# Optimization experiments

Hardware: AMD Instinct MI355X
Metric: run time of the kernel (lower is better)

## Reference

```python
import jax, jax.numpy as jnp
import numpy as np

TEMP = 0.7
TOPK_RATIO = 0.75
BN_EPS = 1e-5  # eval-mode BN with running_mean=0, running_var=1


def conv3x3(x, w):
    # x: [N,C,H,W], w: [O,I,3,3], stride 1, pad 1
    return jax.lax.conv_general_dilated(x, w, (1, 1), 'SAME',
                                        dimension_numbers=('NCHW', 'OIHW', 'NCHW'))


def bn(x, g, b):
    scale = g / jnp.sqrt(1.0 + BN_EPS)
    return x * scale[:, None, None] + b[:, None, None]


def glu(x):
    c = x.shape[1] // 2
    return x[:, :c] * jax.nn.sigmoid(x[:, c:])


def resblock(x, w1, g1, b1, w2, g2, b2):
    out = glu(bn(conv3x3(x, w1), g1, b1))
    out = bn(conv3x3(out, w2), g2, b2)
    return out + x


def refined_attention(h_code, word_embs, w_ctx, mask):
    B, C, H, W = h_code.shape
    Q = H * W
    S = word_embs.shape[2]
    # conv_context is a 1x1 conv (no bias): pure channel projection
    sourceT = jnp.einsum('oc,bcs->bos', w_ctx, word_embs)   # [B, idf, S]
    target = h_code.reshape(B, C, Q)                        # [B, idf, Q]
    attn = jnp.einsum('bcq,bcs->bqs', target, sourceT)      # [B, Q, S]
    attn = attn.reshape(B * Q, S) / TEMP
    # faithful to torch: mask.repeat(queryL, 1) tiles mask over rows
    mask_exp = jnp.tile(mask, (Q, 1))                       # [B*Q, S]
    attn = jnp.where(mask_exp, -jnp.inf, attn)
    if TOPK_RATIO < 1.0 and S > 1:
        k = max(1, int(S * TOPK_RATIO))
        topk_vals, _ = jax.lax.top_k(attn, k)               # sorted desc
        threshold = topk_vals[:, -1:]                       # min of top-k
        attn = jnp.where(attn < threshold, -jnp.inf, attn)
    p = jax.nn.softmax(attn, axis=1)
    nan_rows = jnp.any(jnp.isnan(p), axis=1, keepdims=True)
    p = jnp.where(nan_rows, 1.0 / S, p)                     # uniform fallback
    p = p.reshape(B, Q, S)
    attn_t = jnp.swapaxes(p, 1, 2)                          # [B, S, Q]
    wctx = jnp.einsum('bos,bsq->boq', sourceT, attn_t).reshape(B, C, H, W)
    att_map = attn_t.reshape(B, S, H, W)
    return wctx, att_map


def upsample2x(x):
    return jnp.repeat(jnp.repeat(x, 2, axis=2), 2, axis=3)


def reference(h_code, c_code, word_embs, w_ctx,
              r0_w1, r0_g1, r0_b1, r0_w2, r0_g2, r0_b2,
              r1_w1, r1_g1, r1_b1, r1_w2, r1_g2, r1_b2,
              up_w, up_g, up_b, mask):
    # c_code is in the signature of NEXT_STAGE_G.forward but unused (as in AttnGAN)
    c_code_att, att = refined_attention(h_code, word_embs, w_ctx, mask)
    h_c = jnp.concatenate([h_code, c_code_att], axis=1)     # [B, 2*ngf, H, W]
    out = resblock(h_c, r0_w1, r0_g1, r0_b1, r0_w2, r0_g2, r0_b2)
    out = resblock(out, r1_w1, r1_g1, r1_b1, r1_w2, r1_g2, r1_b2)
    # upBlock: nearest upsample x2 -> conv3x3(2ngf, 2ngf) -> BN -> GLU -> ngf
    out = glu(bn(conv3x3(upsample2x(out), up_w), up_g, up_b))
    return out, att


def setup_inputs() -> dict:
    key = jax.random.key(0)
    ks = jax.random.split(key, 24)
    B, ngf, H, W = 8, 64, 128, 128
    nef, ncf, S = 256, 100, 32
    C2 = 2 * ngf  # 128
    std = 0.02
    inp = {
        'h_code': jax.random.normal(ks[0], (B, ngf, H, W), jnp.float32),
        'c_code': jax.random.normal(ks[1], (B, ncf), jnp.float32),
        'word_embs': jax.random.normal(ks[2], (B, nef, S), jnp.float32),
        'mask': jax.random.randint(ks[3], (B, S), 0, 2).astype(bool),
        'w_ctx': jax.random.normal(ks[4], (ngf, nef), jnp.float32) * std,
    }
    for i, base in enumerate([5, 11]):
        inp[f'r{i}_w1'] = jax.random.normal(ks[base + 0], (2 * C2, C2, 3, 3), jnp.float32) * std
        inp[f'r{i}_g1'] = jnp.ones((2 * C2,), jnp.float32)
        inp[f'r{i}_b1'] = jnp.zeros((2 * C2,), jnp.float32)
        inp[f'r{i}_w2'] = jax.random.normal(ks[base + 3], (C2, C2, 3, 3), jnp.float32) * std
        inp[f'r{i}_g2'] = jnp.ones((C2,), jnp.float32)
        inp[f'r{i}_b2'] = jnp.zeros((C2,), jnp.float32)
    inp['up_w'] = jax.random.normal(ks[17], (2 * ngf, C2, 3, 3), jnp.float32) * std
    inp['up_g'] = jnp.ones((2 * ngf,), jnp.float32)
    inp['up_b'] = jnp.zeros((2 * ngf,), jnp.float32)
    return inp
```

## Files before the change

### kernel.cpp

```cpp
#include <hip/hip_runtime.h>
#include <math.h>


#define B_N 8
#define NGF 64
#define HC 128
#define WC 128
#define QN (HC*WC)
#define NEF 256
#define SN 32
#define TEMP_INV (1.0f/0.7f)
#define BN_SC 0.99999500003749969f
#define TOPK 24

typedef _Float16 f16;
typedef __attribute__((ext_vector_type(8))) _Float16 f16x8;
typedef __attribute__((ext_vector_type(4))) _Float16 f16x4;
typedef __attribute__((ext_vector_type(4))) float f32x4;

__device__ __forceinline__ void gload16(const void* g, void* l) {
    __builtin_amdgcn_global_load_lds(
        (const __attribute__((address_space(1))) void*)g,
        (__attribute__((address_space(3))) void*)l,
        16, 0, 0);
}

__global__ void prep_mask_k(const void* __restrict__ mraw,
                            unsigned* __restrict__ mbits,
                            unsigned* __restrict__ zp) {
    __shared__ int mode;
    if (threadIdx.x == 0) {
        const unsigned* u = (const unsigned*)mraw;
        bool i32 = true, f32m = true;
        for (int i = 0; i < 64; ++i) {
            unsigned v = u[i];
            if (v > 1u) i32 = false;
            if (v != 0u && v != 0x3F800000u) f32m = false;
        }
        mode = i32 ? 0 : (f32m ? 1 : 2);
    }
    __syncthreads();
    int t = threadIdx.x;
    if (t < 64) zp[(t >> 4) * 262144 + (t & 15)] = 0u;
    if (t < B_N) {
        unsigned bits = 0;
        for (int s = 0; s < SN; ++s) {
            int idx = t * SN + s;
            bool on;
            if (mode == 0)      on = ((const int*)mraw)[idx] != 0;
            else if (mode == 1) on = ((const float*)mraw)[idx] != 0.0f;
            else                on = ((const unsigned char*)mraw)[idx] != 0;
            if (on) bits |= (1u << s);
        }
        mbits[t] = bits;
    }
}

__global__ __launch_bounds__(256) void source_t_k(
        const float* __restrict__ w_ctx, const float* __restrict__ word_embs,
        float* __restrict__ sT) {
    int b = blockIdx.x >> 3;
    int o = ((blockIdx.x & 7) << 3) + (threadIdx.x >> 5);
    int s = threadIdx.x & 31;
    const float* wrow = w_ctx + (size_t)o * NEF;
    const float* wb = word_embs + (size_t)b * NEF * SN + s;
    float acc = 0.0f;
    #pragma unroll 8
    for (int c = 0; c < NEF; ++c) acc += wrow[c] * wb[(size_t)c * SN];
    sT[((size_t)b * NGF + o) * SN + s] = acc;
}

__global__ __launch_bounds__(256) void attention_k(
        const float* __restrict__ h_code, const float* __restrict__ sT,
        const unsigned* __restrict__ mbits,
        float* __restrict__ att_out,
        f16* __restrict__ hc) {
    int r0 = blockIdx.x * 256;
    int b = r0 >> 14;
    __shared__ float st[NGF * SN];
    const float* stg = sT + (size_t)b * NGF * SN;
    for (int i = threadIdx.x; i < NGF * SN; i += 256) st[i] = stg[i];
    __syncthreads();
    int q = (r0 & (QN - 1)) + threadIdx.x;

    const float* hb = h_code + (size_t)b * NGF * QN + q;
    f16* hcb = hc + (size_t)b * QN * 128;

    float a[SN];
    #pragma unroll
    for (int s = 0; s < SN; ++s) a[s] = 0.0f;
    for (int g8 = 0; g8 < 8; ++g8) {
        f16x8 t;
        #pragma unroll
        for (int r = 0; r < 8; ++r) {
            float v = hb[(size_t)(g8 * 8 + r) * QN];
            t[r] = (f16)v;
            #pragma unroll
            for (int s = 0; s < SN; ++s) a[s] += v * st[(g8 * 8 + r) * SN + s];
        }
        *(f16x8*)(hcb + ((size_t)g8 * QN + q) * 8) = t;
    }
    unsigned mb = mbits[q & 7];
    #pragma unroll
    for (int s = 0; s < SN; ++s)
        a[s] = ((mb >> s) & 1u) ? -INFINITY : a[s] * TEMP_INV;

    float thr = -INFINITY;
    #pragma unroll
    for (int s = 0; s < SN; ++s) {
        int rank = 0;
        #pragma unroll
        for (int j = 0; j < SN; ++j)
            rank += (a[j] > a[s]) || (a[j] == a[s] && j < s);
        if (rank == TOPK - 1) thr = a[s];
    }
    float m = -INFINITY;
    #pragma unroll
    for (int s = 0; s < SN; ++s) {
        if (a[s] < thr) a[s] = -INFINITY;
        m = fmaxf(m, a[s]);
    }
    float p[SN];
    if (m == -INFINITY) {
        #pragma unroll
        for (int s = 0; s < SN; ++s) p[s] = 1.0f / SN;
    } else {
        float sum = 0.0f;
        #pragma unroll
        for (int s = 0; s < SN; ++s) { p[s] = __expf(a[s] - m); sum += p[s]; }
        float inv = 1.0f / sum;
        #pragma unroll
        for (int s = 0; s < SN; ++s) p[s] *= inv;
    }
    float* ao = att_out + (size_t)b * SN * QN + q;
    #pragma unroll
    for (int s = 0; s < SN; ++s) ao[(size_t)s * QN] = p[s];
    for (int g8 = 0; g8 < 8; ++g8) {
        f16x8 t;
        #pragma unroll
        for (int r = 0; r < 8; ++r) {
            float acc = 0.0f;
            #pragma unroll
            for (int s = 0; s < SN; ++s) acc += st[(g8 * 8 + r) * SN + s] * p[s];
            t[r] = (f16)acc;
        }
        *(f16x8*)(hcb + ((size_t)(8 + g8) * QN + q) * 8) = t;
    }
}

__global__ __launch_bounds__(256) void wt_transform_k(
        const float* __restrict__ w, f16* __restrict__ wt,
        int total, int HALF ) {
    int idx = blockIdx.x * 256 + threadIdx.x;
    if (idx >= total) return;
    int e   = idx & 7;
    int gp  = (idx >> 3) & 3;
    int cop = (idx >> 5) & 63;
    int u   = idx >> 11;
    int t   = u % 9;
    int v   = u / 9;
    int cc  = v & 3;
    int cb  = v >> 2;
    int g   = gp ^ ((cop >> 1) & 3);
    int ci  = cc * 32 + g * 8 + e;
    int co  = HALF ? (cop < 32 ? cb * 32 + cop : HALF + cb * 32 + (cop - 32))
                   : cb * 64 + cop;
    wt[idx] = (f16)w[((size_t)co * 128 + ci) * 9 + t];
}

__global__ __launch_bounds__(256) void wt_up_transform_k(
        const float* __restrict__ w, f16* __restrict__ wt) {
    int idx = blockIdx.x * 256 + threadIdx.x;
    int e   = idx & 7;
    int gp  = (idx >> 3) & 3;
    int cop = (idx >> 5) & 63;
    int tap = (idx >> 11) & 3;
    int pw  = (idx >> 13) & 1;
    int cc  = (idx >> 14) & 3;
    int ph  = (idx >> 16) & 1;
    int cb  = (idx >> 17) & 1;
    int g   = gp ^ ((cop >> 1) & 3);
    int ci  = cc * 32 + g * 8 + e;
    int co  = cop < 32 ? cb * 32 + cop : 64 + cb * 32 + (cop - 32);
    int ra = tap >> 1, bb = tap & 1;
    const float* wp = w + ((size_t)co * 128 + ci) * 9;
    float acc = 0.0f;
    #pragma unroll
    for (int kh = 0; kh < 3; ++kh) {
        int rma = (ph == 0) ? (kh == 0 ? 0 : 1) : (kh == 2 ? 1 : 0);
        if (rma != ra) continue;
        #pragma unroll
        for (int kw = 0; kw < 3; ++kw) {
            int cma = (pw == 0) ? (kw == 0 ? 0 : 1) : (kw == 2 ? 1 : 0);
            if (cma == bb) acc += wp[kh * 3 + kw];
        }
    }
    wt[idx] = (f16)acc;
}

template<int COUT, bool GLU, bool RES>
__global__ __launch_bounds__(512) void conv_mfma_k(
        const f16* __restrict__ in, const f16* __restrict__ wt,
        const float* __restrict__ gamma, const float* __restrict__ beta,
        const f16* __restrict__ res, f16* __restrict__ outh,
        const char* __restrict__ zeros) {
    constexpr int HALF = COUT / 2;
    constexpr int OCH  = GLU ? HALF : COUT;
    constexpr int IBUF = 57344;

    __shared__ char smem[2 * IBUF + 36864];
    char* wB = smem + 2 * IBUF;

    const int tid = threadIdx.x, lane = tid & 63, wv = tid >> 6;
    const int l15 = lane & 15, kg = lane >> 4;
    const int b = blockIdx.z, cb = blockIdx.y, qt = blockIdx.x;
    const int q0 = qt * 512;
    const int h0 = qt * 4;
    const int lr = wv >> 1, chf = wv & 1;

    f32x4 acc[4][4];
    #pragma unroll
    for (int m = 0; m < 4; ++m)
        #pragma unroll
        for (int n = 0; n < 4; ++n) acc[m][n] = (f32x4){0.f, 0.f, 0.f, 0.f};

    const f16* inb = in + (size_t)b * QN * 128;
    const char* wtb = (const char*)wt + (size_t)cb * 147456;

    const char* srcK[7];
    #pragma unroll
    for (int k = 0; k < 7; ++k) {
        int idx = (k << 9) + tid;
        int r = idx / 520;
        int rem = idx - r * 520;
        int wi = rem >> 2, gp = rem & 3;
        int g = gp ^ ((wi >> 1) & 3);
        int gh = h0 - 1 + r;
        int gw = wi - 1;
        const char* s = zeros;
        if (r < 6 && (unsigned)gh < (unsigned)HC && (unsigned)gw < (unsigned)WC)
            s = (const char*)(inb + (((size_t)g * QN + (size_t)gh * WC + gw) << 3));
        srcK[k] = s;
    }
    const int dstB = (tid & 448) << 4;

    auto stage_in = [&](int cc, int buf) {
        char* base = smem + buf * IBUF;
        #pragma unroll
        for (int k = 0; k < 7; ++k)
            gload16(srcK[k] + (cc << 20), base + (k << 13) + dstB);
    };
    auto stage_w = [&](int cc) {
        const char* wsrc = wtb + cc * 36864 + (tid << 4);
        #pragma unroll
        for (int k = 0; k < 4; ++k)
            gload16(wsrc + (k << 13), wB + (k << 13) + dstB);
        if (tid < 256)
            gload16(wsrc + (4 << 13), wB + (4 << 13) + dstB);
    };

    stage_in(0, 0);
    stage_w(0);
    __syncthreads();
    for (int cc = 0; cc < 4; ++cc) {
        if (cc < 3) stage_in(cc + 1, (cc + 1) & 1);
        const char* bb = smem + (cc & 1) * IBUF;

        #pragma unroll
        for (int t = 0; t < 9; ++t) {
            const int kh = t / 3, kw = t % 3;
            f16x8 af[4], bf[4];
            #pragma unroll
            for (int m = 0; m < 4; ++m) {
                int co = m * 16 + l15;
                af[m] = *(const f16x8*)(wB + (t << 12) + (co << 6)
                                        + ((kg ^ ((co >> 1) & 3)) << 4));
            }
            #pragma unroll
            for (int n = 0; n < 4; ++n) {
                int wi = chf * 64 + (n << 4) + l15 + kw;
                int off = (lr + kh) * 8320 + wi * 64 + ((kg ^ ((wi >> 1) & 3)) << 4);
                bf[n] = *(const f16x8*)(bb + off);
            }
            #pragma unroll
            for (int m = 0; m < 4; ++m)
                #pragma unroll
                for (int n = 0; n < 4; ++n)
                    acc[m][n] = __builtin_amdgcn_mfma_f32_16x16x32_f16(af[m], bf[n], acc[m][n], 0, 0, 0);
        }
        __syncthreads();
        if (cc < 3) {
            stage_w(cc + 1);
            __syncthreads();
        }
    }

    const int r4 = kg * 4;
    const int qb = lr * 128 + chf * 64;
    if (GLU) {
        #pragma unroll
        for (int mv = 0; mv < 2; ++mv) {
            const int v0 = cb * 32 + mv * 16 + r4;
            float s1[4], o1[4], s2[4], o2[4];
            #pragma unroll
            for (int r = 0; r < 4; ++r) {
                s1[r] = gamma[v0 + r] * BN_SC;        o1[r] = beta[v0 + r];
                s2[r] = gamma[v0 + r + HALF] * BN_SC; o2[r] = beta[v0 + r + HALF];
            }
            #pragma unroll
            for (int n = 0; n < 4; ++n) {
                const int qc = qb + (n << 4) + l15;
                float ov[4];
                #pragma unroll
                for (int r = 0; r < 4; ++r) {
                    float yv = acc[mv][n][r] * s1[r] + o1[r];
                    float zv = acc[mv + 2][n][r] * s2[r] + o2[r];
                    ov[r] = yv / (1.0f + __expf(-zv));
                }
                f16x4 tv;
                #pragma unroll
                for (int r = 0; r < 4; ++r) tv[r] = (f16)ov[r];
                *(f16x4*)(outh + ((((size_t)b * (OCH / 8) + (v0 >> 3)) << 14)
                                  + q0 + qc) * 8 + (v0 & 7)) = tv;
            }
        }
    } else {
        #pragma unroll
        for (int m = 0; m < 4; ++m) {
            const int c0 = cb * 64 + m * 16 + r4;
            float s[4], o[4];
            #pragma unroll
            for (int r = 0; r < 4; ++r) {
                s[r] = gamma[c0 + r] * BN_SC; o[r] = beta[c0 + r];
            }
            #pragma unroll
            for (int n = 0; n < 4; ++n) {
                const int qc = qb + (n << 4) + l15;
                const size_t gaddr = ((((size_t)b * 16 + (c0 >> 3)) << 14) + q0 + qc) * 8 + (c0 & 7);
                float ov[4];
                #pragma unroll
                for (int r = 0; r < 4; ++r) ov[r] = acc[m][n][r] * s[r] + o[r];
                if (RES) {
                    f16x4 rv = *(const f16x4*)(res + gaddr);
                    #pragma unroll
                    for (int r = 0; r < 4; ++r) ov[r] += (float)rv[r];
                }
                f16x4 tv;
                #pragma unroll
                for (int r = 0; r < 4; ++r) tv[r] = (f16)ov[r];
                *(f16x4*)(outh + gaddr) = tv;
            }
        }
    }
}

__global__ __launch_bounds__(512, 2) void conv_up_k(
        const f16* __restrict__ in, const f16* __restrict__ wt,
        const float* __restrict__ gamma, const float* __restrict__ beta,
        float* __restrict__ outf, const char* __restrict__ zeros) {
    constexpr int HIN = 128, WIN = 128;
    constexpr int INB = 41600;
    constexpr int BUFB = INB + 32768;
    __shared__ char smem[2 * BUFB];

    const int tid = threadIdx.x, lane = tid & 63, wv = tid >> 6;
    const int l15 = lane & 15, kg = lane >> 4;
    const int b = blockIdx.z, cb = blockIdx.y;
    const int j = blockIdx.x >> 1, ph = blockIdx.x & 1;
    const int rr = wv >> 1;
    const int p  = wv & 1;

    f32x4 acc[4][8];
    #pragma unroll
    for (int m = 0; m < 4; ++m)
        #pragma unroll
        for (int n = 0; n < 8; ++n) acc[m][n] = (f32x4){0.f, 0.f, 0.f, 0.f};

    const f16* inb = in + (size_t)b * HIN * WIN * 128;
    const char* wtb = (const char*)wt + (size_t)(cb * 2 + ph) * 131072;

    const char* srcK[6];
    #pragma unroll
    for (int k = 0; k < 6; ++k) {
        int idx = (k < 5) ? ((k << 9) + tid) : (2560 + tid);
        int r = idx / 520;
        int rem = idx - r * 520;
        int wi = rem >> 2, gp = rem & 3;
        int g = gp ^ ((wi >> 1) & 3);
        int sh = 4 * j - 1 + ph + r;
        int sw = wi - 1;
        const char* s = zeros;
        if (r < 5 && (unsigned)sh < (unsigned)HIN && (unsigned)sw < (unsigned)WIN)
            s = (const char*)(inb + (((size_t)g * (HIN * WIN) + (size_t)sh * WIN + sw) << 3));
        srcK[k] = s;
    }
    const int dstB = (tid & 448) << 4;

    auto stage = [&](int cc, int buf) {
        char* base = smem + buf * BUFB;
        #pragma unroll
        for (int k = 0; k < 5; ++k)
            gload16(srcK[k] + (cc << 20), base + (k << 13) + dstB);
        if (tid < 40)
            gload16(srcK[5] + (cc << 20), base + 40960);
        const char* wsrc = wtb + cc * 32768 + (tid << 4);
        #pragma unroll
        for (int k = 0; k < 4; ++k)
            gload16(wsrc + (k << 13), base + INB + (k << 13) + dstB);
    };

    stage(0, 0);
    __syncthreads();
    for (int cc = 0; cc < 4; ++cc) {
        if (cc < 3) stage(cc + 1, (cc + 1) & 1);
        const char* bb = smem + (cc & 1) * BUFB;
        const char* wB = bb + INB;

        #pragma unroll
        for (int t = 0; t < 4; ++t) {
            f16x8 af[4], bf[8];
            const int tapbase = (p * 4 + t) << 12;
            #pragma unroll
            for (int m = 0; m < 4; ++m) {
                int co = m * 16 + l15;
                af[m] = *(const f16x8*)(wB + tapbase + (co << 6)
                                        + ((kg ^ ((co >> 1) & 3)) << 4));
            }
            #pragma unroll
            for (int n = 0; n < 8; ++n) {
                int si = (n << 4) + l15 + (t & 1) + p;
                int off = (rr + (t >> 1)) * 8320 + si * 64
                          + ((kg ^ ((si >> 1) & 3)) << 4);
                bf[n] = *(const f16x8*)(bb + off);
            }
            #pragma unroll
            for (int m = 0; m < 4; ++m)
                #pragma unroll
                for (int n = 0; n < 8; ++n)
                    acc[m][n] = __builtin_amdgcn_mfma_f32_16x16x32_f16(af[m], bf[n], acc[m][n], 0, 0, 0);
        }
        __syncthreads();
    }

    const int r4 = kg * 4;
    const int h = 8 * j + 2 * rr + ph;
    #pragma unroll
    for (int mv = 0; mv < 2; ++mv) {
        const int v0 = cb * 32 + mv * 16 + r4;
        float s1[4], o1[4], s2[4], o2[4];
        #pragma unroll
        for (int r = 0; r < 4; ++r) {
            s1[r] = gamma[v0 + r] * BN_SC;      o1[r] = beta[v0 + r];
            s2[r] = gamma[v0 + r + 64] * BN_SC; o2[r] = beta[v0 + r + 64];
        }
        #pragma unroll
        for (int n = 0; n < 8; ++n) {
            const int w = 2 * ((n << 4) + l15) + p;
            float ov[4];
            #pragma unroll
            for (int r = 0; r < 4; ++r) {
                float yv = acc[mv][n][r] * s1[r] + o1[r];
                float zv = acc[mv + 2][n][r] * s2[r] + o2[r];
                ov[r] = yv / (1.0f + __expf(-zv));
            }
            #pragma unroll
            for (int r = 0; r < 4; ++r)
                outf[(((size_t)b * 64 + v0 + r) * 256 + h) * 256 + w] = ov[r];
        }
    }
}

extern "C" void kernel_launch(void* const* d_in, const int* in_sizes, int n_in,
                              void* d_out, int out_size, void* d_ws, size_t ws_size,
                              hipStream_t stream) {
    (void)in_sizes; (void)n_in; (void)out_size; (void)ws_size;
    const float* h_code    = (const float*)d_in[0];
    const float* word_embs = (const float*)d_in[2];
    const void*  mask      = d_in[3];
    const float* w_ctx     = (const float*)d_in[4];
    const float* r0_w1 = (const float*)d_in[5];
    const float* r0_g1 = (const float*)d_in[6];
    const float* r0_b1 = (const float*)d_in[7];
    const float* r0_w2 = (const float*)d_in[8];
    const float* r0_g2 = (const float*)d_in[9];
    const float* r0_b2 = (const float*)d_in[10];
    const float* r1_w1 = (const float*)d_in[11];
    const float* r1_g1 = (const float*)d_in[12];
    const float* r1_b1 = (const float*)d_in[13];
    const float* r1_w2 = (const float*)d_in[14];
    const float* r1_g2 = (const float*)d_in[15];
    const float* r1_b2 = (const float*)d_in[16];
    const float* up_w  = (const float*)d_in[17];
    const float* up_g  = (const float*)d_in[18];
    const float* up_b  = (const float*)d_in[19];

    float* outp = (float*)d_out;
    float* attp = outp + (size_t)B_N * NGF * 4 * HC * WC;

    unsigned* mbits = (unsigned*)d_ws;
    float* sT  = (float*)((char*)d_ws + 1024);
    char* zeros = (char*)d_ws + ((size_t)4 << 20);
    f16* hcA   = (f16*)((char*)d_ws + ((size_t)8 << 20));
    f16* wtbuf = (f16*)((char*)d_ws + ((size_t)40 << 20));

    const int W1_TOT = 4 * 4 * 9 * 64 * 32;
    const int W2_TOT = 2 * 4 * 9 * 64 * 32;
    const int WUP_TOT = 2 * 2 * 4 * 2 * 4 * 64 * 32;
    f16* Wr0c1 = wtbuf;
    f16* Wr0c2 = Wr0c1 + W1_TOT;
    f16* Wr1c1 = Wr0c2 + W2_TOT;
    f16* Wr1c2 = Wr1c1 + W1_TOT;
    f16* Wup   = Wr1c2 + W2_TOT;

    f16* Bbuf = (f16*)d_out;
    f16* Cbuf = (f16*)((char*)d_out + ((size_t)32 << 20));

    prep_mask_k<<<1, 64, 0, stream>>>(mask, mbits, (unsigned*)zeros);
    source_t_k<<<64, 256, 0, stream>>>(w_ctx, word_embs, sT);

    wt_transform_k<<<(W1_TOT + 255) / 256, 256, 0, stream>>>(r0_w1, Wr0c1, W1_TOT, 128);
    wt_transform_k<<<(W2_TOT + 255) / 256, 256, 0, stream>>>(r0_w2, Wr0c2, W2_TOT, 0);
    wt_transform_k<<<(W1_TOT + 255) / 256, 256, 0, stream>>>(r1_w1, Wr1c1, W1_TOT, 128);
    wt_transform_k<<<(W2_TOT + 255) / 256, 256, 0, stream>>>(r1_w2, Wr1c2, W2_TOT, 0);
    wt_up_transform_k<<<WUP_TOT / 256, 256, 0, stream>>>(up_w, Wup);

    attention_k<<<(B_N * QN) / 256, 256, 0, stream>>>(h_code, sT, mbits, attp, hcA);

    conv_mfma_k<256, true,  false>
        <<<dim3(32, 4, B_N), 512, 0, stream>>>(hcA, Wr0c1, r0_g1, r0_b1, nullptr, Bbuf, zeros);
    conv_mfma_k<128, false, true>
        <<<dim3(32, 2, B_N), 512, 0, stream>>>(Bbuf, Wr0c2, r0_g2, r0_b2, hcA, Cbuf, zeros);
    conv_mfma_k<256, true,  false>
        <<<dim3(32, 4, B_N), 512, 0, stream>>>(Cbuf, Wr1c1, r1_g1, r1_b1, nullptr, Bbuf, zeros);
    conv_mfma_k<128, false, true>
        <<<dim3(32, 2, B_N), 512, 0, stream>>>(Bbuf, Wr1c2, r1_g2, r1_b2, Cbuf, hcA, zeros);
    conv_up_k<<<dim3(64, 2, B_N), 512, 0, stream>>>(hcA, Wup, up_g, up_b, outp, zeros);
}
```

Before: 410.5 us.

## Load upsample-conv activations directly from global into registers, keep weights resident in LDS

The upsample conv kernel no longer stages input tiles through double-buffered shared memory. It loads all 128KB of weights into LDS once, then reads activation fragments straight from global memory into registers, software-pipelined one tap ahead. The zero-padding buffer initialisation is enlarged so out-of-range rows and columns read zeros. This removes per-chunk LDS staging and barriers, but relies on cache hits for the overlapping activation reads. The 128KB LDS allocation also limits occupancy, possibly to one block per CU despite the launch bounds of 2.

```diff
diff --git a/kernel.cpp b/kernel.cpp
--- a/kernel.cpp
+++ b/kernel.cpp
@@ -41,7 +41,10 @@
     }
     __syncthreads();
     int t = threadIdx.x;
-    if (t < 64) zp[(t >> 4) * 262144 + (t & 15)] = 0u;
+    for (int i = t; i < 4 * 1056; i += 256) {
+        int cc = i / 1056, w = i - cc * 1056;
+        zp[cc * 262144 + w - 16] = 0u;
+    }
     if (t < B_N) {
         unsigned bits = 0;
         for (int s = 0; s < SN; ++s) {
@@ -358,10 +361,7 @@
         const f16* __restrict__ in, const f16* __restrict__ wt,
         const float* __restrict__ gamma, const float* __restrict__ beta,
         float* __restrict__ outf, const char* __restrict__ zeros) {
-    constexpr int HIN = 128, WIN = 128;
-    constexpr int INB = 41600;
-    constexpr int BUFB = INB + 32768;
-    __shared__ char smem[2 * BUFB];
+    __shared__ char wL[131072];
 
     const int tid = threadIdx.x, lane = tid & 63, wv = tid >> 6;
     const int l15 = lane & 15, kg = lane >> 4;
@@ -370,76 +370,79 @@
     const int rr = wv >> 1;
     const int p  = wv & 1;
 
+    const char* wtb = (const char*)wt + (size_t)(cb * 2 + ph) * 131072;
+    const int dstB = (tid & 448) << 4;
+    #pragma unroll
+    for (int k = 0; k < 16; ++k)
+        gload16(wtb + (((k << 9) + tid) << 4), wL + (k << 13) + dstB);
+    __syncthreads();
+
     f32x4 acc[4][8];
     #pragma unroll
     for (int m = 0; m < 4; ++m)
         #pragma unroll
         for (int n = 0; n < 8; ++n) acc[m][n] = (f32x4){0.f, 0.f, 0.f, 0.f};
 
-    const f16* inb = in + (size_t)b * HIN * WIN * 128;
-    const char* wtb = (const char*)wt + (size_t)(cb * 2 + ph) * 131072;
-
-    const char* srcK[6];
-    #pragma unroll
-    for (int k = 0; k < 6; ++k) {
-        int idx = (k < 5) ? ((k << 9) + tid) : (2560 + tid);
-        int r = idx / 520;
-        int rem = idx - r * 520;
-        int wi = rem >> 2, gp = rem & 3;
-        int g = gp ^ ((wi >> 1) & 3);
-        int sh = 4 * j - 1 + ph + r;
-        int sw = wi - 1;
-        const char* s = zeros;
-        if (r < 5 && (unsigned)sh < (unsigned)HIN && (unsigned)sw < (unsigned)WIN)
-            s = (const char*)(inb + (((size_t)g * (HIN * WIN) + (size_t)sh * WIN + sw) << 3));
-        srcK[k] = s;
-    }
-    const int dstB = (tid & 448) << 4;
-
-    auto stage = [&](int cc, int buf) {
-        char* base = smem + buf * BUFB;
-        #pragma unroll
-        for (int k = 0; k < 5; ++k)
-            gload16(srcK[k] + (cc << 20), base + (k << 13) + dstB);
-        if (tid < 40)
-            gload16(srcK[5] + (cc << 20), base + 40960);
-        const char* wsrc = wtb + cc * 32768 + (tid << 4);
-        #pragma unroll
-        for (int k = 0; k < 4; ++k)
-            gload16(wsrc + (k << 13), base + INB + (k << 13) + dstB);
+    const char* inbB = (const char*)in + (size_t)b * QN * 256;
+    const int colb = (l15 + p - 1) << 4;
+    const char* rp0;
+    const char* rp1;
+    {
+        int r0 = 4 * j - 1 + ph + rr;
+        int r1 = r0 + 1;
+        rp0 = ((unsigned)r0 < 128u)
+            ? inbB + (((size_t)kg * QN + (size_t)r0 * 128) << 4) + colb
+            : zeros + 16 + colb;
+        rp1 = ((unsigned)r1 < 128u)
+            ? inbB + (((size_t)kg * QN + (size_t)r1 * 128) << 4) + colb
+            : zeros + 16 + colb;
+    }
+
+    auto LG = [&](f16x8 (&bf)[8], int cc, int t) {
+        const int sh_ = t & 1;
+        const char* bl = ((t >> 1) ? rp1 : rp0) + (cc << 20) + (sh_ << 4);
+        #pragma unroll
+        for (int n = 0; n < 8; ++n) {
+            if (n == 0 || n == 7) {
+                int sc = (n << 4) + l15 + sh_ + p - 1;
+                const char* a = ((unsigned)sc < 128u)
+                    ? (bl + n * 256)
+                    : (zeros + (cc << 20) + 16 + sc * 16);
+                bf[n] = *(const f16x8*)a;
+            } else {
+                bf[n] = *(const f16x8*)(bl + n * 256);
+            }
+        }
     };
-
-    stage(0, 0);
-    __syncthreads();
-    for (int cc = 0; cc < 4; ++cc) {
-        if (cc < 3) stage(cc + 1, (cc + 1) & 1);
-        const char* bb = smem + (cc & 1) * BUFB;
-        const char* wB = bb + INB;
-
-        #pragma unroll
-        for (int t = 0; t < 4; ++t) {
-            f16x8 af[4], bf[8];
-            const int tapbase = (p * 4 + t) << 12;
-            #pragma unroll
-            for (int m = 0; m < 4; ++m) {
-                int co = m * 16 + l15;
-                af[m] = *(const f16x8*)(wB + tapbase + (co << 6)
-                                        + ((kg ^ ((co >> 1) & 3)) << 4));
-            }
-            #pragma unroll
-            for (int n = 0; n < 8; ++n) {
-                int si = (n << 4) + l15 + (t & 1) + p;
-                int off = (rr + (t >> 1)) * 8320 + si * 64
-                          + ((kg ^ ((si >> 1) & 3)) << 4);
-                bf[n] = *(const f16x8*)(bb + off);
-            }
-            #pragma unroll
-            for (int m = 0; m < 4; ++m)
-                #pragma unroll
-                for (int n = 0; n < 8; ++n)
-                    acc[m][n] = __builtin_amdgcn_mfma_f32_16x16x32_f16(af[m], bf[n], acc[m][n], 0, 0, 0);
-        }
-        __syncthreads();
+    auto CP = [&](f16x8 (&bf)[8], int cc, int t) {
+        f16x8 af[4];
+        const int tb = cc * 32768 + ((p * 4 + t) << 12);
+        #pragma unroll
+        for (int m = 0; m < 4; ++m) {
+            int co = m * 16 + l15;
+            af[m] = *(const f16x8*)(wL + tb + (co << 6)
+                                    + ((kg ^ ((co >> 1) & 3)) << 4));
+        }
+        #pragma unroll
+        for (int m = 0; m < 4; ++m)
+            #pragma unroll
+            for (int n = 0; n < 8; ++n)
+                acc[m][n] = __builtin_amdgcn_mfma_f32_16x16x32_f16(af[m], bf[n], acc[m][n], 0, 0, 0);
+    };
+
+    f16x8 bfA[8], bfB[8];
+    LG(bfA, 0, 0);
+    #pragma unroll
+    for (int k = 0; k < 16; ++k) {
+        const int cc = k >> 2, t = k & 3;
+        const int k1 = k + 1;
+        if ((k & 1) == 0) {
+            if (k1 < 16) LG(bfB, k1 >> 2, k1 & 3);
+            CP(bfA, cc, t);
+        } else {
+            if (k1 < 16) LG(bfA, k1 >> 2, k1 & 3);
+            CP(bfB, cc, t);
+        }
     }
 
     const int r4 = kg * 4;
@@ -515,7 +518,7 @@
     f16* Bbuf = (f16*)d_out;
     f16* Cbuf = (f16*)((char*)d_out + ((size_t)32 << 20));
 
-    prep_mask_k<<<1, 64, 0, stream>>>(mask, mbits, (unsigned*)zeros);
+    prep_mask_k<<<1, 256, 0, stream>>>(mask, mbits, (unsigned*)zeros);
     source_t_k<<<64, 256, 0, stream>>>(w_ctx, word_embs, sT);
 
     wt_transform_k<<<(W1_TOT + 255) / 256, 256, 0, stream>>>(r0_w1, Wr0c1, W1_TOT, 128);
```

Result: no change. 405.1 us (-1.3%).
